# Kernel optimization log

Hardware: AMD Instinct MI355X
Metric: run time of the kernel (lower is better)

The kernel has to match this reference:

```python
import jax, jax.numpy as jnp
import numpy as np

NQ, NS, D, DC, HT = 100000, 2000, 128, 64, 128
B, T = 128, 500
NNZ_HG, NNZ_GCN, NNZ_SIM = 300000, 64000, 1000000
NUM_MV, NUM_QL = 2, 2


def spmm(rows, cols, vals, x, n_rows):
    # y = A @ x, A sparse COO with A[rows[k], cols[k]] = vals[k]
    return jax.ops.segment_sum(vals[:, None] * x[cols], rows, num_segments=n_rows)


def gcn_conv(x, src, dst, W, b, n):
    # PyG-style GCNConv: sym-normalized (A + I), then linear + bias
    h = x @ W
    loop = jnp.arange(n, dtype=src.dtype)
    s = jnp.concatenate([src, loop])
    d = jnp.concatenate([dst, loop])
    deg = jax.ops.segment_sum(jnp.ones(s.shape[0], jnp.float32), d, num_segments=n)
    dinv = jax.lax.rsqrt(jnp.maximum(deg, 1.0))
    norm = dinv[s] * dinv[d]
    return jax.ops.segment_sum(norm[:, None] * h[s], d, num_segments=n) + b


def setup_inputs() -> dict:
    key = jax.random.key(0)
    ks = iter(jax.random.split(key, 64))
    nrm = lambda shape, s=0.05: jax.random.normal(next(ks), shape, jnp.float32) * s
    ri = lambda shape, hi: jax.random.randint(next(ks), shape, 0, hi, jnp.int32)
    inp = {}
    inp['question_seq'] = ri((B, T), NQ)
    inp['skill_seq'] = ri((B, T), NS)
    inp['answer_seq'] = ri((B, T), 2)
    inp['hg_q'] = ri((NNZ_HG,), NQ)
    inp['hg_c'] = ri((NNZ_HG,), NS)
    inp['gcn_src'] = ri((NNZ_GCN,), NS)
    inp['gcn_dst'] = ri((NNZ_GCN,), NS)
    inp['sim_src'] = ri((NNZ_SIM,), NQ)
    inp['sim_dst'] = ri((NNZ_SIM,), NQ)
    inp['hg_vals_qc'] = jax.random.uniform(next(ks), (NNZ_HG,), jnp.float32) * 0.05
    inp['hg_vals_cq'] = jax.random.uniform(next(ks), (NNZ_HG,), jnp.float32) * 0.05
    inp['sim_vals'] = jax.random.uniform(next(ks), (NNZ_SIM,), jnp.float32) * 0.02
    inp['q_emb'] = nrm((NQ + 1, D))
    inp['s_emb'] = nrm((NS + 1, D))
    inp['c_emb'] = nrm((3, DC))
    for nm in ['w_g1', 'w_g2', 'w_g3']:
        inp[nm] = nrm((D, D))
    for nm in ['b_g1', 'b_g2', 'b_g3']:
        inp[nm] = nrm((1, D))
    for i in [1, 2, 3]:
        inp['gcn_w%d' % i] = nrm((D, D))
        inp['gcn_b%d' % i] = nrm((D,))
    for nm in ['w_sg1', 'w_sg2', 'w_qg1', 'w_qg3']:
        inp[nm] = nrm((D, 1))
    for nm in ['b_sg1', 'b_sg2', 'b_qg1', 'b_qg3']:
        inp[nm] = nrm((1,))
    LIN = 2 * D + DC
    inp['w_ih'] = nrm((4 * HT, LIN))
    inp['w_hh'] = nrm((4 * HT, HT))
    inp['b_ih'] = nrm((4 * HT,))
    inp['b_hh'] = nrm((4 * HT,))
    inp['fc1_w'] = nrm((HT + 2 * D, HT))
    inp['fc1_b'] = nrm((HT,))
    inp['fc2_w'] = nrm((HT, 1))
    inp['fc2_b'] = nrm((1,))
    return inp


def reference(question_seq, skill_seq, answer_seq, hg_q, hg_c, gcn_src, gcn_dst,
              sim_src, sim_dst, hg_vals_qc, hg_vals_cq, sim_vals,
              q_emb, s_emb, c_emb, w_g1, w_g2, w_g3, b_g1, b_g2, b_g3,
              gcn_w1, gcn_b1, gcn_w2, gcn_b2, gcn_w3, gcn_b3,
              w_sg1, w_sg2, w_qg1, w_qg3, b_sg1, b_sg2, b_qg1, b_qg3,
              w_ih, w_hh, b_ih, b_hh, fc1_w, fc1_b, fc2_w, fc2_b):
    sig = jax.nn.sigmoid
    # gated (channel-specific) embedding tables, excluding padding row
    one_gate = s_emb[:-1] * sig(s_emb[:-1] @ w_g1 + b_g1)
    two_gate = s_emb[:-1] * sig(s_emb[:-1] @ w_g2 + b_g2)
    three_gate = q_emb[:-1] * sig(q_emb[:-1] @ w_g3 + b_g3)

    # channel 1: multi-view hypergraph conv with residual + mean over layers (dropout p=0 -> identity)
    embs = [one_gate]
    x = one_gate
    for _ in range(NUM_MV):
        m = spmm(hg_q, hg_c, hg_vals_qc, x, NQ)   # HG_qc @ x -> [NQ, D]
        x = spmm(hg_c, hg_q, hg_vals_cq, m, NS)   # HG_cq @ m -> [NS, D]
        x = x + embs[-1]
        embs.append(x)
    one_skill = jnp.mean(jnp.stack(embs), 0)
    one_q = spmm(hg_q, hg_c, hg_vals_qc, one_skill, NQ)  # structural question embs
    one_skill_p = jnp.concatenate([one_skill, s_emb[-1:]], 0)
    one_q_p = jnp.concatenate([one_q, q_emb[-1:]], 0)
    one_b_skill = one_skill_p[skill_seq]   # [B,T,D]
    one_b_q = one_q_p[question_seq]        # [B,T,D]

    # channel 2: 3-layer GCN with relu (dropout p=0)
    x = jax.nn.relu(gcn_conv(two_gate, gcn_src, gcn_dst, gcn_w1, gcn_b1, NS))
    x = jax.nn.relu(gcn_conv(x, gcn_src, gcn_dst, gcn_w2, gcn_b2, NS))
    x = jax.nn.relu(gcn_conv(x, gcn_src, gcn_dst, gcn_w3, gcn_b3, NS))
    two_skill_p = jnp.concatenate([x, s_emb[-1:]], 0)
    two_b_skill = two_skill_p[skill_seq]

    # channel 3: question similarity conv with residual + mean over layers
    embs = [three_gate]
    x = three_gate
    for _ in range(NUM_QL):
        x = spmm(sim_src, sim_dst, sim_vals, x, NQ) + embs[-1]
        embs.append(x)
    three_q = jnp.mean(jnp.stack(embs), 0)
    three_q_p = jnp.concatenate([three_q, q_emb[-1:]], 0)
    three_b_q = three_q_p[question_seq]

    # gated channel fusion
    fused_skill = sig(one_b_skill @ w_sg1 + b_sg1) * one_b_skill \
                + sig(two_b_skill @ w_sg2 + b_sg2) * two_b_skill
    fused_q = sig(one_b_q @ w_qg1 + b_qg1) * one_b_q \
            + sig(three_b_q @ w_qg3 + b_qg3) * three_b_q
    corr = c_emb[answer_seq]  # [B,T,DC]
    lstm_in = jnp.concatenate([fused_q, fused_skill, corr], -1)  # [B,T,2D+DC]

    def step(carry, xt):
        h, c = carry
        z = xt @ w_ih.T + b_ih + h @ w_hh.T + b_hh
        i, f, g, o = jnp.split(z, 4, axis=-1)  # torch LSTM gate order
        c = sig(f) * c + sig(i) * jnp.tanh(g)
        h = sig(o) * jnp.tanh(c)
        return (h, c), h

    b = lstm_in.shape[0]
    h0 = jnp.zeros((b, HT), lstm_in.dtype)
    _, hs = jax.lax.scan(step, (h0, h0), jnp.swapaxes(lstm_in, 0, 1))
    hs = jnp.swapaxes(hs, 0, 1)  # [B,T,HT]

    pred_in = jnp.concatenate([hs, fused_q, fused_skill], -1)  # [B,T,HT+2D]
    preds = sig(jax.nn.relu(pred_in @ fc1_w + fc1_b) @ fc2_w + fc2_b)  # [B,T,1]
    return preds
```

## Files before the change

kernel.cpp:

```cpp
#include <hip/hip_runtime.h>

#define NQc 100000
#define NSc 2000
#define Dc 128
#define DCc 64
#define HTc 128
#define Bc 128
#define Tc 500
#define BTc (Bc*Tc)
#define NNZ_HGc 300000
#define NNZ_GCNc 64000
#define NNZ_SIMc 1000000
#define LINc 320
#define G4c 512

using bf16x8  = __attribute__((ext_vector_type(8))) short;
using floatx4 = __attribute__((ext_vector_type(4))) float;
typedef _Float16 half2v __attribute__((ext_vector_type(2)));

__device__ __forceinline__ float sigf(float x){ return 1.0f/(1.0f + __expf(-x)); }
__device__ __forceinline__ float tanhfast(float x){ return 2.0f*sigf(2.0f*x) - 1.0f; }

__device__ __forceinline__ unsigned short bf16r(float x){
  unsigned u = __float_as_uint(x);
// ... 10 lines not shown
  #pragma unroll
  for (int off=32; off>0; off>>=1) v += __shfl_xor(v, off, 64);
  return v;
}

__global__ void fill_kernel(float* p, float v, int n){
  int i = blockIdx.x*blockDim.x + threadIdx.x;
  if (i<n) p[i] = v;
}

__global__ void cvt_bf16_kernel(const float* __restrict__ in, unsigned short* __restrict__ out, long n){
  long i = (long)blockIdx.x*blockDim.x + threadIdx.x;
  long stride = (long)gridDim.x*blockDim.x;
  for (; i<n; i+=stride) out[i] = bf16r(in[i]);
}
__global__ void cvtT_bf16_kernel(const float* __restrict__ in, unsigned short* __restrict__ out, int R, int C){
  int i = blockIdx.x*blockDim.x + threadIdx.x;
  if (i < R*C){ int r = i/C, c = i%C; out[(size_t)c*R + r] = bf16r(in[i]); }
}
__global__ void cvt_f16_kernel(const float* __restrict__ in, _Float16* __restrict__ out, int n){
  int i = blockIdx.x*blockDim.x + threadIdx.x;
  if (i<n) out[i] = (_Float16)in[i];
}
__global__ void cvtP_wih_kernel(const float* __restrict__ in, unsigned short* __restrict__ out){
  int i = blockIdx.x*blockDim.x + threadIdx.x;
  if (i < G4c*LINc){
    int r = i/LINc, c = i%LINc;
    int rp = (r&127)*4 + (r>>7);
    out[(size_t)rp*LINc + c] = bf16r(in[i]);
  }
}
__global__ void biasP_kernel(const float* __restrict__ bih, const float* __restrict__ bhh, float* __restrict__ out){
  int r = blockIdx.x*blockDim.x + threadIdx.x;
  if (r < G4c) out[(r&127)*4 + (r>>7)] = bih[r] + bhh[r];
}

__global__ void hist_kernel(const int* __restrict__ rows, int* cnt, int nnz){
  int i = blockIdx.x*blockDim.x + threadIdx.x;
  int stride = gridDim.x*blockDim.x;
  for (; i<nnz; i+=stride) atomicAdd(&cnt[rows[i]], 1);
}

__global__ __launch_bounds__(1024) void scan_local_kernel(const int* __restrict__ cnt, int* __restrict__ rowptr,
                                                          int* __restrict__ bsum, int n){
  __shared__ int buf[1024];
  int tid = threadIdx.x;
  int i = blockIdx.x*1024 + tid;
  int v = (i<n) ? cnt[i] : 0;
  buf[tid] = v;
  __syncthreads();
  for (int off=1; off<1024; off<<=1){
    int t = (tid>=off) ? buf[tid-off] : 0;
    __syncthreads();
    buf[tid] += t;
    __syncthreads();
  }
  if (i<n) rowptr[i] = buf[tid] - v;
  if (tid==1023) bsum[blockIdx.x] = buf[1023];
}
__global__ __launch_bounds__(128) void scan_bsum_kernel(int* bsum, int nb){
  __shared__ int s[128];
  int tid = threadIdx.x;
  int v = (tid<nb) ? bsum[tid] : 0;
  s[tid] = v;
  __syncthreads();
  for (int off=1; off<128; off<<=1){
    int t = (tid>=off) ? s[tid-off] : 0;
    __syncthreads();
    s[tid] += t;
    __syncthreads();
  }
  if (tid<nb) bsum[tid] = s[tid] - v;
  if (tid==0) bsum[nb] = s[127];
}
__global__ void scan_add_kernel(int* rowptr, int* cur, const int* __restrict__ bsum, int n, int nb){
  int i = blockIdx.x*blockDim.x + threadIdx.x;
  if (i<n){ int r = rowptr[i] + bsum[i>>10]; rowptr[i]=r; cur[i]=r; }
  if (i==0) rowptr[n] = bsum[nb];
}

__global__ void scatter_kernel(const int* __restrict__ rows, const int* __restrict__ cols,
                               const float* __restrict__ vals, int* cur,
                               int* col_out, float* val_out, int nnz){
  int i = blockIdx.x*blockDim.x + threadIdx.x;
  int stride = gridDim.x*blockDim.x;
  for (; i<nnz; i+=stride){
    int r = rows[i];
    int p = atomicAdd(&cur[r], 1);
    col_out[p] = cols[i];
    if (vals) val_out[p] = vals[i];
  }
}

__global__ void dinv_kernel(const int* __restrict__ cnt, float* dinv, int n){
  int i = blockIdx.x*blockDim.x + threadIdx.x;
  if (i<n) dinv[i] = rsqrtf((float)cnt[i] + 1.0f);
}

__global__ void copy_kernel(float* __restrict__ dst, const float* __restrict__ src, long n4){
  long i = (long)blockIdx.x*blockDim.x + threadIdx.x;
  long stride = (long)gridDim.x*blockDim.x;
  const float4* s = (const float4*)src; float4* d = (float4*)dst;
  for (; i<n4; i+=stride) d[i] = s[i];
}

#define BM 64
#define BN 64
#define BK 16
__global__ __launch_bounds__(256) void gemm_kernel(
    const float* __restrict__ A, int lda,
    const float* __restrict__ Bm, float* __restrict__ C,
    const float* __restrict__ bias, const float* __restrict__ gsrc,
    int M, int N, int K, int ep)
{
  __shared__ float As[BM][BK+4];
  __shared__ float Bs[BK][BN+4];
  int tid = threadIdx.x;
  int tx = tid & 15, ty = tid >> 4;
  int mBase = blockIdx.y*BM, nBase = blockIdx.x*BN;
  float acc[4][4];
  #pragma unroll
  for (int i=0;i<4;i++)
    #pragma unroll
    for (int j=0;j<4;j++) acc[i][j]=0.f;
  int arow = tid>>2, ac4 = tid&3;
  for (int kt=0; kt<K; kt+=BK){
// ... 19 lines not shown
      acc[3][0]+=a3*b0; acc[3][1]+=a3*b1; acc[3][2]+=a3*b2; acc[3][3]+=a3*b3;
    }
    __syncthreads();
  }
  #pragma unroll
  for (int i=0;i<4;i++){
    int m = mBase + ty*4 + i;
    if (m >= M) continue;
    #pragma unroll
    for (int j=0;j<4;j++){
      int n = nBase + tx*4 + j;
      float v = acc[i][j];
      if (bias)  v += bias[n];
      if (ep==1)      v = gsrc[(size_t)m*N + n] * sigf(v);
      C[(size_t)m*N + n] = v;
    }
  }
}

__global__ __launch_bounds__(256) void mfma_gemm_kernel(
    const unsigned short* __restrict__ A1, int lda1,
    const unsigned short* __restrict__ A2, int lda2, int ksplit,
    const unsigned short* __restrict__ Bt,
    float* __restrict__ C, unsigned short* __restrict__ Cbf,
    const float* __restrict__ bias, const float* __restrict__ bias2,
    const float* __restrict__ gsrc,
    int M, int N, int K, int ep)
{
  __shared__ unsigned short Asm[128*64];
  __shared__ unsigned short Bsm[128*64];
  int tid = threadIdx.x;
  int wave = tid>>6, lane = tid&63;
  int quad = lane>>4, l16 = lane&15;
  int m0 = blockIdx.y*128, n0 = blockIdx.x*128;
  int wm = (wave&1)*64, wn = (wave>>1)*64;
  floatx4 acc[4][4];
  #pragma unroll
  for (int i=0;i<4;i++)
    #pragma unroll
    for (int j=0;j<4;j++) acc[i][j] = (floatx4){0.f,0.f,0.f,0.f};

  for (int kt=0; kt<K; kt+=64){
    #pragma unroll
    for (int i=0;i<4;i++){
      int idx = i*256 + tid;
// ... 24 lines not shown
      }
      #pragma unroll
      for (int nt=0;nt<4;nt++){
        int row = wn + nt*16 + l16;
        int blk = ks*4 + quad;
        bfr[nt] = *(const bf16x8*)&Bsm[row*64 + ((blk ^ (row&7))<<3)];
      }
      #pragma unroll
      for (int mt=0;mt<4;mt++)
        #pragma unroll
        for (int nt=0;nt<4;nt++)
          acc[mt][nt] = __builtin_amdgcn_mfma_f32_16x16x32_bf16(af[mt], bfr[nt], acc[mt][nt], 0,0,0);
    }
    __syncthreads();
  }
  #pragma unroll
  for (int mt=0;mt<4;mt++){
    #pragma unroll
    for (int nt=0;nt<4;nt++){
      int col = n0 + wn + nt*16 + l16;
      #pragma unroll
      for (int r=0;r<4;r++){
        int row = m0 + wm + mt*16 + quad*4 + r;
        if (row < M){
          float v = acc[mt][nt][r];
          if (bias)  v += bias[col];
          if (bias2) v += bias2[col];
          if (ep==1)      v = gsrc[(size_t)row*N + col] * sigf(v);
          else if (ep==2) v = fmaxf(v, 0.f);
          C[(size_t)row*N + col] = v;
          if (Cbf) Cbf[(size_t)row*N + col] = bf16r(v);
        }
      }
    }
  }
}

__global__ __launch_bounds__(256) void spmm_bf_kernel(
    const int* __restrict__ rowptr, const int* __restrict__ col, const float* __restrict__ val,
    const unsigned short* __restrict__ xbf, const float* __restrict__ resid,
    const float* __restrict__ resid2, float beta,
    float* __restrict__ y, unsigned short* __restrict__ ybf, float* __restrict__ sumbuf,
    float alpha, int nrows)
{
  int w = (int)((blockIdx.x*(unsigned)blockDim.x + threadIdx.x) >> 6);
  int lane = threadIdx.x & 63;
  if (w >= nrows) return;
  int beg = rowptr[w], end = rowptr[w+1];
  const unsigned* x2 = (const unsigned*)xbf;
  float ax=0.f, ay=0.f;
  int k = beg;
  for (; k+4 <= end; k+=4){
    int c0=col[k], c1=col[k+1], c2=col[k+2], c3=col[k+3];
    float v0=val[k], v1=val[k+1], v2=val[k+2], v3=val[k+3];
    unsigned u0 = x2[(size_t)c0*64 + lane];
    unsigned u1 = x2[(size_t)c1*64 + lane];
    unsigned u2 = x2[(size_t)c2*64 + lane];
// ... 6 lines not shown
  for (; k<end; k++){
    int c = col[k]; float v = val[k];
    unsigned u = x2[(size_t)c*64 + lane];
    ax += v*bflo(u); ay += v*bfhi(u);
  }
  ax*=alpha; ay*=alpha;
  if (resid){ float2 r = ((const float2*)resid)[(size_t)w*64+lane]; ax+=r.x; ay+=r.y; }
  if (resid2){ float2 r = ((const float2*)resid2)[(size_t)w*64+lane]; ax+=beta*r.x; ay+=beta*r.y; }
  float2 o; o.x=ax; o.y=ay;
  ((float2*)y)[(size_t)w*64+lane] = o;
  if (ybf) ((unsigned*)ybf)[(size_t)w*64+lane] = pack2(o);
  if (sumbuf){
    float2 s = ((float2*)sumbuf)[(size_t)w*64+lane];
    s.x+=ax; s.y+=ay;
    ((float2*)sumbuf)[(size_t)w*64+lane] = s;
  }
}

__global__ __launch_bounds__(256) void gcn_spmm_kernel(
    const int* __restrict__ rowptr, const int* __restrict__ src, const float* __restrict__ dinv,
    const float* __restrict__ h, const float* __restrict__ bias, float* __restrict__ out, int nrows)
{
  int w = (int)((blockIdx.x*(unsigned)blockDim.x + threadIdx.x) >> 6);
  int lane = threadIdx.x & 63;
  if (w >= nrows) return;
  int beg = rowptr[w], end = rowptr[w+1];
  const float2* h2 = (const float2*)h;
  float dr = dinv[w];
  float2 self = h2[(size_t)w*64+lane];
  float ax = dr*self.x, ay = dr*self.y;
// ... 68 lines not shown
  rowb[lane]      = pack2(fq);
  rowb[64 + lane] = pack2(fs);
  if (lane < 32){
    float2 cv = ((const float2*)(c_emb + (size_t)a*DCc))[lane];
    rowb[128 + lane] = pack2(cv);
  }
}

__global__ __launch_bounds__(512, 2) void lstm_kernel(
    const float* __restrict__ xpart, const _Float16* __restrict__ w_hh_h,
    unsigned short* __restrict__ hs_bf)
{
  __shared__ __align__(16) _Float16 h_lds[2][HTc];
  int b = blockIdx.x, tid = threadIdx.x;
  int j = tid >> 2, sub = tid & 3;
  half2v w[4][16];
  #pragma unroll
  for (int g=0; g<4; g++){
    const half2v* wp = (const half2v*)(w_hh_h + (size_t)(g*128 + j)*HTc + sub*32);
    #pragma unroll
    for (int i=0;i<16;i++) w[g][i] = wp[i];
  }
  if (tid < HTc) h_lds[0][tid] = (_Float16)0.f;
  float c = 0.f;
  __syncthreads();
  const float* xp = xpart + (size_t)b*Tc*G4c;
  unsigned short* hb = hs_bf + (size_t)b*Tc*HTc;
  float xcur = xp[tid];
  for (int t=0; t<Tc; t++){
    int tn = (t+1 < Tc) ? t+1 : Tc-1;
    float xnext = xp[(size_t)tn*G4c + tid];
    int cur = t & 1;
    float4 hv[4];
    const float4* hsrc = (const float4*)&h_lds[cur][sub*32];
    #pragma unroll
    for (int i=0;i<4;i++) hv[i] = hsrc[i];
    const half2v* hh = (const half2v*)hv;
    float p0=0.f,p1=0.f,p2=0.f,p3=0.f;
    #pragma unroll
    for (int i=0;i<16;i++){
#if __has_builtin(__builtin_amdgcn_fdot2)
      p0 = __builtin_amdgcn_fdot2(w[0][i], hh[i], p0, false);
      p1 = __builtin_amdgcn_fdot2(w[1][i], hh[i], p1, false);
      p2 = __builtin_amdgcn_fdot2(w[2][i], hh[i], p2, false);
      p3 = __builtin_amdgcn_fdot2(w[3][i], hh[i], p3, false);
#else
      p0 += (float)w[0][i].x*(float)hh[i].x + (float)w[0][i].y*(float)hh[i].y;
      p1 += (float)w[1][i].x*(float)hh[i].x + (float)w[1][i].y*(float)hh[i].y;
      p2 += (float)w[2][i].x*(float)hh[i].x + (float)w[2][i].y*(float)hh[i].y;
      p3 += (float)w[3][i].x*(float)hh[i].x + (float)w[3][i].y*(float)hh[i].y;
#endif
    }
    if (sub==0) p0 += xcur; else if (sub==1) p1 += xcur; else if (sub==2) p2 += xcur; else p3 += xcur;
    p0 += __shfl_xor(p0,1); p0 += __shfl_xor(p0,2);
    p1 += __shfl_xor(p1,1); p1 += __shfl_xor(p1,2);
    p2 += __shfl_xor(p2,1); p2 += __shfl_xor(p2,2);
    p3 += __shfl_xor(p3,1); p3 += __shfl_xor(p3,2);
    float ig=sigf(p0), fg=sigf(p1), gg=tanhfast(p2), og=sigf(p3);
    c = fg*c + ig*gg;
    float h = og*tanhfast(c);
    if (sub == 0){
      h_lds[1-cur][j] = (_Float16)h;
      hb[(size_t)t*HTc + j] = bf16r(h);
    }
    __syncthreads();
    xcur = xnext;
  }
}

__global__ __launch_bounds__(256) void final_kernel(
    const float* __restrict__ h1, const float* __restrict__ fc2_w,
    const float* __restrict__ fc2_b, float* __restrict__ out){
  int idx = (int)((blockIdx.x*(unsigned)blockDim.x + threadIdx.x) >> 6);
  int lane = threadIdx.x & 63;
  if (idx >= BTc) return;
  float2 h = ((const float2*)(h1 + (size_t)idx*HTc))[lane];
  float2 w = ((const float2*)fc2_w)[lane];
  float p = wredsum(h.x*w.x + h.y*w.y);
  if (lane==0) out[idx] = sigf(p + fc2_b[0]);
}

extern "C" void kernel_launch(void* const* d_in, const int* in_sizes, int n_in,
                              void* d_out, int out_size, void* d_ws, size_t ws_size,
                              hipStream_t stream)
{
  const int* question_seq=(const int*)d_in[0];
  const int* skill_seq   =(const int*)d_in[1];
  const int* answer_seq  =(const int*)d_in[2];
  const int* hg_q        =(const int*)d_in[3];
  const int* hg_c        =(const int*)d_in[4];
  const int* gcn_src     =(const int*)d_in[5];
  const int* gcn_dst     =(const int*)d_in[6];
  const int* sim_src     =(const int*)d_in[7];
  const int* sim_dst     =(const int*)d_in[8];
// ... 63 lines not shown
  size_t p_val_sim = pall((size_t)NNZ_SIMc*4);
  size_t p_col_hgq = pall((size_t)NNZ_HGc*4);
  size_t p_val_hgq = pall((size_t)NNZ_HGc*4);
  size_t p_col_hgc = pall((size_t)NNZ_HGc*4);
  size_t p_val_hgc = pall((size_t)NNZ_HGc*4);
  size_t p_src_gcn = pall((size_t)NNZ_GCNc*4);
  size_t p_rp_sim  = pall((size_t)(NQc+1)*4);
  size_t p_rp_hgq  = pall((size_t)(NQc+1)*4);
  size_t p_rp_hgc  = pall((size_t)(NSc+1)*4);
  size_t p_rp_gcn  = pall((size_t)(NSc+1)*4);
  size_t p_cnt_sim = pall((size_t)NQc*4);
  size_t p_cnt_hgq = pall((size_t)NQc*4);
  size_t p_cnt_hgc = pall((size_t)NSc*4);
  size_t p_cnt_gcn = pall((size_t)NSc*4);
  size_t p_cnt_end = poff;
  size_t p_bsum    = pall((size_t)130*4);
  size_t p_dinv    = pall((size_t)NSc*4);
  size_t p_onegate = pall((size_t)NSc*Dc*4);
  size_t p_twogate = pall((size_t)NSc*Dc*4);
  size_t p_ssum    = pall((size_t)NSc*Dc*4);
  size_t p_sxA     = pall((size_t)NSc*Dc*4);
  size_t p_sxB     = pall((size_t)NSc*Dc*4);
  size_t p_gxA     = pall((size_t)NSc*Dc*4);
  size_t p_gxB     = pall((size_t)NSc*Dc*4);
  size_t p_htmp    = pall((size_t)NSc*Dc*4);
  size_t p_ogbf    = pall((size_t)NSc*Dc*2);
  size_t p_sxBbf   = pall((size_t)NSc*Dc*2);
  size_t p_ssumbf  = pall((size_t)NSc*Dc*2);
  if (poff > XPbytes){
    fill_kernel<<<(out_size+255)/256, 256, 0, stream>>>(outp, -2.0f, out_size);
    return;
// ... 19 lines not shown
  int*   bsum    = (int*)(xp + p_bsum);
  float* dinv    = (float*)(xp + p_dinv);
  float* one_gate= (float*)(xp + p_onegate);
  float* two_gate= (float*)(xp + p_twogate);
  float* ssum    = (float*)(xp + p_ssum);
  float* sxA     = (float*)(xp + p_sxA);
  float* sxB     = (float*)(xp + p_sxB);
  float* gxA     = (float*)(xp + p_gxA);
  float* gxB     = (float*)(xp + p_gxB);
  float* htmp    = (float*)(xp + p_htmp);
  unsigned short* og_bf   = (unsigned short*)(xp + p_ogbf);
  unsigned short* sxB_bf  = (unsigned short*)(xp + p_sxBbf);
  unsigned short* ssum_bf = (unsigned short*)(xp + p_ssumbf);

  float* xpart   = (float*)xp;
  float* h1buf   = (float*)xp;
  unsigned short* lstm_in_bf = (unsigned short*)(base + o_libf);
  unsigned short* hs_bf      = (unsigned short*)(base + o_hsbf);
  unsigned short* q_emb_bf   = (unsigned short*)(base + o_qembbf);
  unsigned short* bfX        = (unsigned short*)(base + o_qembbf);
  unsigned short* bfY        = (unsigned short*)(base + o_bfY);
  unsigned short* w_ih_bf    = (unsigned short*)(base + o_wihbf);
  unsigned short* fc1_wT     = (unsigned short*)(base + o_fc1wT);
  unsigned short* w_g3T      = (unsigned short*)(base + o_wg3T);
  _Float16*       w_hh_h     = (_Float16*)(base + o_whhh);
  float*          biasP      = (float*)(base + o_biasP);

  auto gemm32 = [&](const float* A, int lda, const float* Bp, float* Cp, const float* bias,
                    const float* gsrc, int M, int N, int K, int ep){
    dim3 g(N/64, (M+63)/64), b(256);
    gemm_kernel<<<g, b, 0, stream>>>(A, lda, Bp, Cp, bias, gsrc, M, N, K, ep);
  };
  auto spmm = [&](const int* rp, const int* col, const float* val, const unsigned short* xb,
                  const float* resid, const float* resid2, float beta,
                  float* y, unsigned short* yb, float* sum, float alpha, int nrows){
    spmm_bf_kernel<<<(nrows+3)/4, 256, 0, stream>>>(rp, col, val, xb, resid, resid2, beta, y, yb, sum, alpha, nrows);
  };
  auto scan = [&](int* cnt, int* rowptr, int n){
    int nb = (n + 1023)/1024;
    scan_local_kernel<<<nb, 1024, 0, stream>>>(cnt, rowptr, bsum, n);
    scan_bsum_kernel<<<1, 128, 0, stream>>>(bsum, nb);
    scan_add_kernel<<<(n+255)/256, 256, 0, stream>>>(rowptr, cnt, bsum, n, nb);
  };

  hipMemsetAsync(xp + p_cnt_sim, 0, p_cnt_end - p_cnt_sim, stream);
  hist_kernel<<<1024, 256, 0, stream>>>(sim_src, cnt_sim, NNZ_SIMc);
  hist_kernel<<<1024, 256, 0, stream>>>(hg_q,    cnt_hgq, NNZ_HGc);
  hist_kernel<<<1024, 256, 0, stream>>>(hg_c,    cnt_hgc, NNZ_HGc);
  hist_kernel<<<256,  256, 0, stream>>>(gcn_dst, cnt_gcn, NNZ_GCNc);
  dinv_kernel<<<(NSc+255)/256, 256, 0, stream>>>(cnt_gcn, dinv, NSc);
  scan(cnt_sim, rp_sim, NQc);
  scan(cnt_hgq, rp_hgq, NQc);
  scan(cnt_hgc, rp_hgc, NSc);
  scan(cnt_gcn, rp_gcn, NSc);
  scatter_kernel<<<1024, 256, 0, stream>>>(sim_src, sim_dst, sim_vals, cnt_sim, col_sim, val_sim, NNZ_SIMc);
  scatter_kernel<<<1024, 256, 0, stream>>>(hg_q, hg_c, hg_vals_qc, cnt_hgq, col_hgq, val_hgq, NNZ_HGc);
  scatter_kernel<<<1024, 256, 0, stream>>>(hg_c, hg_q, hg_vals_cq, cnt_hgc, col_hgc, val_hgc, NNZ_HGc);
  scatter_kernel<<<256,  256, 0, stream>>>(gcn_dst, gcn_src, nullptr, cnt_gcn, src_gcn, nullptr, NNZ_GCNc);

  cvt_bf16_kernel<<<2048, 256, 0, stream>>>(q_emb, q_emb_bf, (long)(NQc+1)*Dc);
  cvtP_wih_kernel<<<(G4c*LINc+255)/256, 256, 0, stream>>>(w_ih, w_ih_bf);
  biasP_kernel<<<2, 256, 0, stream>>>(b_ih, b_hh, biasP);
  cvtT_bf16_kernel<<<(384*HTc+255)/256, 256, 0, stream>>>(fc1_w, fc1_wT, 384, HTc);
  cvtT_bf16_kernel<<<(Dc*Dc+255)/256, 256, 0, stream>>>(w_g3, w_g3T, Dc, Dc);
  cvt_f16_kernel<<<(G4c*HTc+255)/256, 256, 0, stream>>>(w_hh, w_hh_h, G4c*HTc);

  {
    dim3 g(1, (NQc+127)/128);
    mfma_gemm_kernel<<<g, 256, 0, stream>>>(q_emb_bf, Dc, q_emb_bf, Dc, Dc, w_g3T,
                                            Abuf, bfY, b_g3, nullptr, q_emb, NQc, Dc, Dc, 1);
  }
  spmm(rp_sim, col_sim, val_sim, bfY, Abuf, nullptr, 0.f, Bbuf, bfX,    nullptr, 1.f, NQc);
  spmm(rp_sim, col_sim, val_sim, bfX, Abuf, Bbuf, 2.f,   Abuf, nullptr, nullptr, 1.f, NQc);

  gemm32(s_emb, Dc, w_g1, one_gate, b_g1, s_emb, NSc, Dc, Dc, 1);
  gemm32(s_emb, Dc, w_g2, two_gate, b_g2, s_emb, NSc, Dc, Dc, 1);
  cvt_bf16_kernel<<<500, 256, 0, stream>>>(one_gate, og_bf, (long)NSc*Dc);

  copy_kernel<<<256, 256, 0, stream>>>(ssum, one_gate, (long)NSc*Dc/4);
  spmm(rp_hgq, col_hgq, val_hgq, og_bf,  nullptr, nullptr, 0.f, Bbuf, bfY,     nullptr, 1.f, NQc);
  spmm(rp_hgc, col_hgc, val_hgc, bfY,    one_gate, nullptr, 0.f, sxB,  sxB_bf,  ssum,    1.f, NSc);
  spmm(rp_hgq, col_hgq, val_hgq, sxB_bf, nullptr, nullptr, 0.f, Bbuf, bfY,     nullptr, 1.f, NQc);
  spmm(rp_hgc, col_hgc, val_hgc, bfY,    sxB,     nullptr, 0.f, sxA,  nullptr, ssum,    1.f, NSc);
  cvt_bf16_kernel<<<500, 256, 0, stream>>>(ssum, ssum_bf, (long)NSc*Dc);
  spmm(rp_hgq, col_hgq, val_hgq, ssum_bf, nullptr, nullptr, 0.f, Bbuf, nullptr, nullptr, 1.f/3.f, NQc);

  gemm32(two_gate, Dc, gcn_w1, htmp, nullptr, nullptr, NSc, Dc, Dc, 0);
  gcn_spmm_kernel<<<(NSc+3)/4, 256, 0, stream>>>(rp_gcn, src_gcn, dinv, htmp, gcn_b1, gxA, NSc);
  gemm32(gxA, Dc, gcn_w2, htmp, nullptr, nullptr, NSc, Dc, Dc, 0);
  gcn_spmm_kernel<<<(NSc+3)/4, 256, 0, stream>>>(rp_gcn, src_gcn, dinv, htmp, gcn_b2, gxB, NSc);
  gemm32(gxB, Dc, gcn_w3, htmp, nullptr, nullptr, NSc, Dc, Dc, 0);
  gcn_spmm_kernel<<<(NSc+3)/4, 256, 0, stream>>>(rp_gcn, src_gcn, dinv, htmp, gcn_b3, gxA, NSc);

  gather_fuse_kernel<<<(BTc+3)/4, 256, 0, stream>>>(
      question_seq, skill_seq, answer_seq,
      ssum, Bbuf, gxA, Abuf,
      s_emb, q_emb, c_emb,
      w_sg1, w_sg2, w_qg1, w_qg3, b_sg1, b_sg2, b_qg1, b_qg3,
      lstm_in_bf);

  {
    dim3 g(G4c/128, BTc/128);
    mfma_gemm_kernel<<<g, 256, 0, stream>>>(lstm_in_bf, LINc, lstm_in_bf, LINc, LINc, w_ih_bf,
                                            xpart, nullptr, biasP, nullptr, nullptr, BTc, G4c, LINc, 0);
  }

  lstm_kernel<<<Bc, 512, 0, stream>>>(xpart, w_hh_h, hs_bf);

  {
    dim3 g(1, BTc/128);
    mfma_gemm_kernel<<<g, 256, 0, stream>>>(hs_bf, HTc, lstm_in_bf, LINc, HTc, fc1_wT,
                                            h1buf, nullptr, fc1_b, nullptr, nullptr, BTc, HTc, 384, 2);
  }
  final_kernel<<<(BTc+3)/4, 256, 0, stream>>>(h1buf, fc2_w, fc2_b, outp);
}
```

Before: 1.503 ms.

## Batch preprocessing kernels, fuse fc2 into fc1 GEMM epilogue, pin LSTM weights

```diff
diff --git a/kernel.cpp b/kernel.cpp
--- a/kernel.cpp
+++ b/kernel.cpp
@@ -48,39 +48,73 @@
   long stride = (long)gridDim.x*blockDim.x;
   for (; i<n; i+=stride) out[i] = bf16r(in[i]);
 }
-__global__ void cvtT_bf16_kernel(const float* __restrict__ in, unsigned short* __restrict__ out, int R, int C){
+
+__global__ void cvt_weights_kernel(
+    const float* __restrict__ w_ih, unsigned short* __restrict__ w_ih_bf,
+    const float* __restrict__ fc1_w, unsigned short* __restrict__ fc1_wT,
+    const float* __restrict__ w_g3, unsigned short* __restrict__ w_g3T,
+    const float* __restrict__ w_hh, _Float16* __restrict__ w_hh_h,
+    const float* __restrict__ b_ih, const float* __restrict__ b_hh, float* __restrict__ biasP)
+{
   int i = blockIdx.x*blockDim.x + threadIdx.x;
-  if (i < R*C){ int r = i/C, c = i%C; out[(size_t)c*R + r] = bf16r(in[i]); }
-}
-__global__ void cvt_f16_kernel(const float* __restrict__ in, _Float16* __restrict__ out, int n){
-  int i = blockIdx.x*blockDim.x + threadIdx.x;
-  if (i<n) out[i] = (_Float16)in[i];
-}
-__global__ void cvtP_wih_kernel(const float* __restrict__ in, unsigned short* __restrict__ out){
-  int i = blockIdx.x*blockDim.x + threadIdx.x;
-  if (i < G4c*LINc){
+  const int T0 = G4c*LINc;
+  const int T1 = T0 + 384*HTc;
+  const int T2 = T1 + Dc*Dc;
+  const int T3 = T2 + G4c*HTc;
+  const int T4 = T3 + G4c;
+  if (i < T0){
     int r = i/LINc, c = i%LINc;
     int rp = (r&127)*4 + (r>>7);
-    out[(size_t)rp*LINc + c] = bf16r(in[i]);
-  }
-}
-__global__ void biasP_kernel(const float* __restrict__ bih, const float* __restrict__ bhh, float* __restrict__ out){
-  int r = blockIdx.x*blockDim.x + threadIdx.x;
-  if (r < G4c) out[(r&127)*4 + (r>>7)] = bih[r] + bhh[r];
-}
-
-__global__ void hist_kernel(const int* __restrict__ rows, int* cnt, int nnz){
-  int i = blockIdx.x*blockDim.x + threadIdx.x;
-  int stride = gridDim.x*blockDim.x;
-  for (; i<nnz; i+=stride) atomicAdd(&cnt[rows[i]], 1);
-}
-
-__global__ __launch_bounds__(1024) void scan_local_kernel(const int* __restrict__ cnt, int* __restrict__ rowptr,
-                                                          int* __restrict__ bsum, int n){
+    w_ih_bf[(size_t)rp*LINc + c] = bf16r(w_ih[i]);
+  } else if (i < T1){
+    int j = i - T0; int r = j/HTc, c = j%HTc;
+    fc1_wT[(size_t)c*384 + r] = bf16r(fc1_w[j]);
+  } else if (i < T2){
+    int j = i - T1; int r = j/Dc, c = j%Dc;
+    w_g3T[(size_t)c*Dc + r] = bf16r(w_g3[j]);
+  } else if (i < T3){
+    int j = i - T2;
+    w_hh_h[j] = (_Float16)w_hh[j];
+  } else if (i < T4){
+    int j = i - T3;
+    biasP[(j&127)*4 + (j>>7)] = b_ih[j] + b_hh[j];
+  }
+}
+
+__global__ void hist_all_kernel(const int* __restrict__ sim_src, int* cnt_sim,
+                                const int* __restrict__ hg_q, int* cnt_hgq,
+                                const int* __restrict__ hg_c, int* cnt_hgc,
+                                const int* __restrict__ gcn_dst, int* cnt_gcn){
+  long i = (long)blockIdx.x*blockDim.x + threadIdx.x;
+  long stride = (long)gridDim.x*blockDim.x;
+  const long T0=NNZ_SIMc, T1=T0+NNZ_HGc, T2=T1+NNZ_HGc, T3=T2+NNZ_GCNc;
+  for (; i<T3; i+=stride){
+    if (i<T0)      atomicAdd(&cnt_sim[sim_src[i]], 1);
+    else if (i<T1) atomicAdd(&cnt_hgq[hg_q[i-T0]], 1);
+    else if (i<T2) atomicAdd(&cnt_hgc[hg_c[i-T1]], 1);
+    else           atomicAdd(&cnt_gcn[gcn_dst[i-T2]], 1);
+  }
+}
+
+#define BS_STRIDE 104
+__global__ __launch_bounds__(1024) void scan_local_all_kernel(
+    const int* __restrict__ cnt_sim, int* rp_sim,
+    const int* __restrict__ cnt_hgq, int* rp_hgq,
+    const int* __restrict__ cnt_hgc, int* rp_hgc,
+    const int* __restrict__ cnt_gcn, int* rp_gcn,
+    int* __restrict__ bsum, float* __restrict__ dinv)
+{
   __shared__ int buf[1024];
-  int tid = threadIdx.x;
-  int i = blockIdx.x*1024 + tid;
+  int b = blockIdx.x, tid = threadIdx.x;
+  const int* cnt; int* rp; int* bs; int n; int lb; int seg;
+  if (b < 98)      { seg=0; cnt=cnt_sim; rp=rp_sim; n=NQc; lb=b; }
+  else if (b <196) { seg=1; cnt=cnt_hgq; rp=rp_hgq; n=NQc; lb=b-98; }
+  else if (b <198) { seg=2; cnt=cnt_hgc; rp=rp_hgc; n=NSc; lb=b-196; }
+  else             { seg=3; cnt=cnt_gcn; rp=rp_gcn; n=NSc; lb=b-198; }
+  bs = bsum + seg*BS_STRIDE;
+  int i = lb*1024 + tid;
   int v = (i<n) ? cnt[i] : 0;
+  if (seg==3 && i<n) dinv[i] = rsqrtf((float)v + 1.0f);
   buf[tid] = v;
   __syncthreads();
   for (int off=1; off<1024; off<<=1){
@@ -89,13 +123,15 @@
     buf[tid] += t;
     __syncthreads();
   }
-  if (i<n) rowptr[i] = buf[tid] - v;
-  if (tid==1023) bsum[blockIdx.x] = buf[1023];
-}
-__global__ __launch_bounds__(128) void scan_bsum_kernel(int* bsum, int nb){
+  if (i<n) rp[i] = buf[tid] - v;
+  if (tid==1023) bs[lb] = buf[1023];
+}
+__global__ __launch_bounds__(128) void scan_bsum_all_kernel(int* bsum){
   __shared__ int s[128];
-  int tid = threadIdx.x;
-  int v = (tid<nb) ? bsum[tid] : 0;
+  int seg = blockIdx.x, tid = threadIdx.x;
+  int nb = (seg<2) ? 98 : 2;
+  int* bs = bsum + seg*BS_STRIDE;
+  int v = (tid<nb) ? bs[tid] : 0;
   s[tid] = v;
   __syncthreads();
   for (int off=1; off<128; off<<=1){
@@ -104,38 +140,53 @@
     s[tid] += t;
     __syncthreads();
   }
-  if (tid<nb) bsum[tid] = s[tid] - v;
-  if (tid==0) bsum[nb] = s[127];
-}
-__global__ void scan_add_kernel(int* rowptr, int* cur, const int* __restrict__ bsum, int n, int nb){
-  int i = blockIdx.x*blockDim.x + threadIdx.x;
-  if (i<n){ int r = rowptr[i] + bsum[i>>10]; rowptr[i]=r; cur[i]=r; }
-  if (i==0) rowptr[n] = bsum[nb];
-}
-
-__global__ void scatter_kernel(const int* __restrict__ rows, const int* __restrict__ cols,
-                               const float* __restrict__ vals, int* cur,
-                               int* col_out, float* val_out, int nnz){
-  int i = blockIdx.x*blockDim.x + threadIdx.x;
-  int stride = gridDim.x*blockDim.x;
-  for (; i<nnz; i+=stride){
-    int r = rows[i];
-    int p = atomicAdd(&cur[r], 1);
-    col_out[p] = cols[i];
-    if (vals) val_out[p] = vals[i];
-  }
-}
-
-__global__ void dinv_kernel(const int* __restrict__ cnt, float* dinv, int n){
-  int i = blockIdx.x*blockDim.x + threadIdx.x;
-  if (i<n) dinv[i] = rsqrtf((float)cnt[i] + 1.0f);
-}
-
-__global__ void copy_kernel(float* __restrict__ dst, const float* __restrict__ src, long n4){
+  if (tid<nb) bs[tid] = s[tid] - v;
+  if (tid==0) bs[nb] = s[127];
+}
+__global__ void scan_add_all_kernel(
+    int* rp_sim, int* cnt_sim, int* rp_hgq, int* cnt_hgq,
+    int* rp_hgc, int* cnt_hgc, int* rp_gcn, int* cnt_gcn,
+    const int* __restrict__ bsum)
+{
+  int b = blockIdx.x, tid = threadIdx.x;
+  int* rp; int* cur; const int* bs; int n; int lb; int nb;
+  if (b < 391)      { rp=rp_sim; cur=cnt_sim; bs=bsum;               n=NQc; lb=b;     nb=98; }
+  else if (b < 782) { rp=rp_hgq; cur=cnt_hgq; bs=bsum+BS_STRIDE;     n=NQc; lb=b-391; nb=98; }
+  else if (b < 790) { rp=rp_hgc; cur=cnt_hgc; bs=bsum+2*BS_STRIDE;   n=NSc; lb=b-782; nb=2; }
+  else              { rp=rp_gcn; cur=cnt_gcn; bs=bsum+3*BS_STRIDE;   n=NSc; lb=b-790; nb=2; }
+  int i = lb*256 + tid;
+  if (i<n){ int r = rp[i] + bs[i>>10]; rp[i]=r; cur[i]=r; }
+  if (lb==0 && tid==0) rp[n] = bs[nb];
+}
+
+__global__ void scatter_all_kernel(
+    const int* __restrict__ sim_src, const int* __restrict__ sim_dst, const float* __restrict__ sim_vals,
+    int* cur_sim, int* col_sim, float* val_sim,
+    const int* __restrict__ hg_q, const int* __restrict__ hg_c,
+    const float* __restrict__ hg_vals_qc, const float* __restrict__ hg_vals_cq,
+    int* cur_hgq, int* col_hgq, float* val_hgq,
+    int* cur_hgc, int* col_hgc, float* val_hgc,
+    const int* __restrict__ gcn_dst, const int* __restrict__ gcn_src,
+    int* cur_gcn, int* src_gcn)
+{
   long i = (long)blockIdx.x*blockDim.x + threadIdx.x;
   long stride = (long)gridDim.x*blockDim.x;
-  const float4* s = (const float4*)src; float4* d = (float4*)dst;
-  for (; i<n4; i+=stride) d[i] = s[i];
+  const long T0=NNZ_SIMc, T1=T0+NNZ_HGc, T2=T1+NNZ_HGc, T3=T2+NNZ_GCNc;
+  for (; i<T3; i+=stride){
+    if (i<T0){
+      int r = sim_src[i]; int p = atomicAdd(&cur_sim[r],1);
+      col_sim[p] = sim_dst[i]; val_sim[p] = sim_vals[i];
+    } else if (i<T1){
+      long j=i-T0; int r = hg_q[j]; int p = atomicAdd(&cur_hgq[r],1);
+      col_hgq[p] = hg_c[j]; val_hgq[p] = hg_vals_qc[j];
+    } else if (i<T2){
+      long j=i-T1; int r = hg_c[j]; int p = atomicAdd(&cur_hgc[r],1);
+      col_hgc[p] = hg_q[j]; val_hgc[p] = hg_vals_cq[j];
+    } else {
+      long j=i-T2; int r = gcn_dst[j]; int p = atomicAdd(&cur_gcn[r],1);
+      src_gcn[p] = gcn_src[j];
+    }
+  }
 }
 
 #define BM 64
@@ -144,6 +195,7 @@
 __global__ __launch_bounds__(256) void gemm_kernel(
     const float* __restrict__ A, int lda,
     const float* __restrict__ Bm, float* __restrict__ C,
+    unsigned short* __restrict__ Cbf, float* __restrict__ Ccopy,
     const float* __restrict__ bias, const float* __restrict__ gsrc,
     int M, int N, int K, int ep)
 {
@@ -193,6 +245,8 @@
       if (bias)  v += bias[n];
       if (ep==1)      v = gsrc[(size_t)m*N + n] * sigf(v);
       C[(size_t)m*N + n] = v;
+      if (Cbf)   Cbf[(size_t)m*N + n] = bf16r(v);
+      if (Ccopy) Ccopy[(size_t)m*N + n] = v;
     }
   }
 }
@@ -204,10 +258,12 @@
     float* __restrict__ C, unsigned short* __restrict__ Cbf,
     const float* __restrict__ bias, const float* __restrict__ bias2,
     const float* __restrict__ gsrc,
+    const float* __restrict__ fc2w, const float* __restrict__ fc2b, float* __restrict__ outp,
     int M, int N, int K, int ep)
 {
   __shared__ unsigned short Asm[128*64];
   __shared__ unsigned short Bsm[128*64];
+  __shared__ float rps[2][128];
   int tid = threadIdx.x;
   int wave = tid>>6, lane = tid&63;
   int quad = lane>>4, l16 = lane&15;
@@ -262,6 +318,32 @@
     }
     __syncthreads();
   }
+  if (ep == 3){
+    float fw[4], fb[4];
+    #pragma unroll
+    for (int nt=0;nt<4;nt++){ int col = wn + nt*16 + l16; fw[nt] = fc2w[col]; fb[nt] = bias[col]; }
+    #pragma unroll
+    for (int mt=0;mt<4;mt++){
+      #pragma unroll
+      for (int r=0;r<4;r++){
+        float s = 0.f;
+        #pragma unroll
+        for (int nt=0;nt<4;nt++){
+          float v = acc[mt][nt][r] + fb[nt];
+          v = fmaxf(v, 0.f);
+          s += v*fw[nt];
+        }
+        s += __shfl_xor(s,1); s += __shfl_xor(s,2); s += __shfl_xor(s,4); s += __shfl_xor(s,8);
+        if (l16 == 0) rps[wave>>1][wm + mt*16 + quad*4 + r] = s;
+      }
+    }
+    __syncthreads();
+    if (tid < 128){
+      int row = m0 + tid;
+      if (row < M) outp[row] = sigf(rps[0][tid] + rps[1][tid] + fc2b[0]);
+    }
+    return;
+  }
   #pragma unroll
   for (int mt=0;mt<4;mt++){
     #pragma unroll
@@ -288,7 +370,8 @@
     const int* __restrict__ rowptr, const int* __restrict__ col, const float* __restrict__ val,
     const unsigned short* __restrict__ xbf, const float* __restrict__ resid,
     const float* __restrict__ resid2, float beta,
-    float* __restrict__ y, unsigned short* __restrict__ ybf, float* __restrict__ sumbuf,
+    float* __restrict__ y, unsigned short* __restrict__ ybf,
+    float* __restrict__ sumbuf, unsigned short* __restrict__ sumbf,
     float alpha, int nrows)
 {
   int w = (int)((blockIdx.x*(unsigned)blockDim.x + threadIdx.x) >> 6);
@@ -325,6 +408,7 @@
     float2 s = ((float2*)sumbuf)[(size_t)w*64+lane];
     s.x+=ax; s.y+=ay;
     ((float2*)sumbuf)[(size_t)w*64+lane] = s;
+    if (sumbf) ((unsigned*)sumbf)[(size_t)w*64+lane] = pack2(s);
   }
 }
 
@@ -423,13 +507,18 @@
   __shared__ __align__(16) _Float16 h_lds[2][HTc];
   int b = blockIdx.x, tid = threadIdx.x;
   int j = tid >> 2, sub = tid & 3;
-  half2v w[4][16];
+  unsigned wbits[4][16];
   #pragma unroll
   for (int g=0; g<4; g++){
-    const half2v* wp = (const half2v*)(w_hh_h + (size_t)(g*128 + j)*HTc + sub*32);
-    #pragma unroll
-    for (int i=0;i<16;i++) w[g][i] = wp[i];
-  }
+    const unsigned* wp = (const unsigned*)(w_hh_h + (size_t)(g*128 + j)*HTc + sub*32);
+    #pragma unroll
+    for (int i=0;i<16;i++) wbits[g][i] = wp[i];
+  }
+  #pragma unroll
+  for (int g=0; g<4; g++)
+    #pragma unroll
+    for (int i=0;i<16;i++)
+      asm volatile("" : "+v"(wbits[g][i]));
   if (tid < HTc) h_lds[0][tid] = (_Float16)0.f;
   float c = 0.f;
   __syncthreads();
@@ -448,16 +537,21 @@
     float p0=0.f,p1=0.f,p2=0.f,p3=0.f;
     #pragma unroll
     for (int i=0;i<16;i++){
+      half2v h2 = hh[i];
 #if __has_builtin(__builtin_amdgcn_fdot2)
-      p0 = __builtin_amdgcn_fdot2(w[0][i], hh[i], p0, false);
-      p1 = __builtin_amdgcn_fdot2(w[1][i], hh[i], p1, false);
-      p2 = __builtin_amdgcn_fdot2(w[2][i], hh[i], p2, false);
-      p3 = __builtin_amdgcn_fdot2(w[3][i], hh[i], p3, false);
+      p0 = __builtin_amdgcn_fdot2(__builtin_bit_cast(half2v, wbits[0][i]), h2, p0, false);
+      p1 = __builtin_amdgcn_fdot2(__builtin_bit_cast(half2v, wbits[1][i]), h2, p1, false);
+      p2 = __builtin_amdgcn_fdot2(__builtin_bit_cast(half2v, wbits[2][i]), h2, p2, false);
+      p3 = __builtin_amdgcn_fdot2(__builtin_bit_cast(half2v, wbits[3][i]), h2, p3, false);
 #else
-      p0 += (float)w[0][i].x*(float)hh[i].x + (float)w[0][i].y*(float)hh[i].y;
-      p1 += (float)w[1][i].x*(float)hh[i].x + (float)w[1][i].y*(float)hh[i].y;
-      p2 += (float)w[2][i].x*(float)hh[i].x + (float)w[2][i].y*(float)hh[i].y;
-      p3 += (float)w[3][i].x*(float)hh[i].x + (float)w[3][i].y*(float)hh[i].y;
+      half2v w0 = __builtin_bit_cast(half2v, wbits[0][i]);
+      half2v w1 = __builtin_bit_cast(half2v, wbits[1][i]);
+      half2v w2 = __builtin_bit_cast(half2v, wbits[2][i]);
+      half2v w3 = __builtin_bit_cast(half2v, wbits[3][i]);
+      p0 += (float)w0.x*(float)h2.x + (float)w0.y*(float)h2.y;
+      p1 += (float)w1.x*(float)h2.x + (float)w1.y*(float)h2.y;
+      p2 += (float)w2.x*(float)h2.x + (float)w2.y*(float)h2.y;
+      p3 += (float)w3.x*(float)h2.x + (float)w3.y*(float)h2.y;
 #endif
     }
     if (sub==0) p0 += xcur; else if (sub==1) p1 += xcur; else if (sub==2) p2 += xcur; else p3 += xcur;
@@ -475,18 +569,6 @@
     __syncthreads();
     xcur = xnext;
   }
-}
-
-__global__ __launch_bounds__(256) void final_kernel(
-    const float* __restrict__ h1, const float* __restrict__ fc2_w,
-    const float* __restrict__ fc2_b, float* __restrict__ out){
-  int idx = (int)((blockIdx.x*(unsigned)blockDim.x + threadIdx.x) >> 6);
-  int lane = threadIdx.x & 63;
-  if (idx >= BTc) return;
-  float2 h = ((const float2*)(h1 + (size_t)idx*HTc))[lane];
-  float2 w = ((const float2*)fc2_w)[lane];
-  float p = wredsum(h.x*w.x + h.y*w.y);
-  if (lane==0) out[idx] = sigf(p + fc2_b[0]);
 }
 
 extern "C" void kernel_launch(void* const* d_in, const int* in_sizes, int n_in,
@@ -580,7 +662,7 @@
   size_t p_cnt_hgc = pall((size_t)NSc*4);
   size_t p_cnt_gcn = pall((size_t)NSc*4);
   size_t p_cnt_end = poff;
-  size_t p_bsum    = pall((size_t)130*4);
+  size_t p_bsum    = pall((size_t)4*BS_STRIDE*4);
   size_t p_dinv    = pall((size_t)NSc*4);
   size_t p_onegate = pall((size_t)NSc*Dc*4);
   size_t p_twogate = pall((size_t)NSc*Dc*4);
@@ -630,7 +712,6 @@
   unsigned short* ssum_bf = (unsigned short*)(xp + p_ssumbf);
 
   float* xpart   = (float*)xp;
-  float* h1buf   = (float*)xp;
   unsigned short* lstm_in_bf = (unsigned short*)(base + o_libf);
   unsigned short* hs_bf      = (unsigned short*)(base + o_hsbf);
   unsigned short* q_emb_bf   = (unsigned short*)(base + o_qembbf);
@@ -642,70 +723,59 @@
   _Float16*       w_hh_h     = (_Float16*)(base + o_whhh);
   float*          biasP      = (float*)(base + o_biasP);
 
-  auto gemm32 = [&](const float* A, int lda, const float* Bp, float* Cp, const float* bias,
+  auto gemm32 = [&](const float* A, int lda, const float* Bp, float* Cp,
+                    unsigned short* Cbf, float* Ccopy, const float* bias,
                     const float* gsrc, int M, int N, int K, int ep){
     dim3 g(N/64, (M+63)/64), b(256);
-    gemm_kernel<<<g, b, 0, stream>>>(A, lda, Bp, Cp, bias, gsrc, M, N, K, ep);
+    gemm_kernel<<<g, b, 0, stream>>>(A, lda, Bp, Cp, Cbf, Ccopy, bias, gsrc, M, N, K, ep);
   };
   auto spmm = [&](const int* rp, const int* col, const float* val, const unsigned short* xb,
                   const float* resid, const float* resid2, float beta,
-                  float* y, unsigned short* yb, float* sum, float alpha, int nrows){
-    spmm_bf_kernel<<<(nrows+3)/4, 256, 0, stream>>>(rp, col, val, xb, resid, resid2, beta, y, yb, sum, alpha, nrows);
+                  float* y, unsigned short* yb, float* sum, unsigned short* sumbf,
+                  float alpha, int nrows){
+    spmm_bf_kernel<<<(nrows+3)/4, 256, 0, stream>>>(rp, col, val, xb, resid, resid2, beta, y, yb, sum, sumbf, alpha, nrows);
   };
-  auto scan = [&](int* cnt, int* rowptr, int n){
-    int nb = (n + 1023)/1024;
-    scan_local_kernel<<<nb, 1024, 0, stream>>>(cnt, rowptr, bsum, n);
-    scan_bsum_kernel<<<1, 128, 0, stream>>>(bsum, nb);
-    scan_add_kernel<<<(n+255)/256, 256, 0, stream>>>(rowptr, cnt, bsum, n, nb);
-  };
 
   hipMemsetAsync(xp + p_cnt_sim, 0, p_cnt_end - p_cnt_sim, stream);
-  hist_kernel<<<1024, 256, 0, stream>>>(sim_src, cnt_sim, NNZ_SIMc);
-  hist_kernel<<<1024, 256, 0, stream>>>(hg_q,    cnt_hgq, NNZ_HGc);
-  hist_kernel<<<1024, 256, 0, stream>>>(hg_c,    cnt_hgc, NNZ_HGc);
-  hist_kernel<<<256,  256, 0, stream>>>(gcn_dst, cnt_gcn, NNZ_GCNc);
-  dinv_kernel<<<(NSc+255)/256, 256, 0, stream>>>(cnt_gcn, dinv, NSc);
-  scan(cnt_sim, rp_sim, NQc);
-  scan(cnt_hgq, rp_hgq, NQc);
-  scan(cnt_hgc, rp_hgc, NSc);
-  scan(cnt_gcn, rp_gcn, NSc);
-  scatter_kernel<<<1024, 256, 0, stream>>>(sim_src, sim_dst, sim_vals, cnt_sim, col_sim, val_sim, NNZ_SIMc);
-  scatter_kernel<<<1024, 256, 0, stream>>>(hg_q, hg_c, hg_vals_qc, cnt_hgq, col_hgq, val_hgq, NNZ_HGc);
-  scatter_kernel<<<1024, 256, 0, stream>>>(hg_c, hg_q, hg_vals_cq, cnt_hgc, col_hgc, val_hgc, NNZ_HGc);
-  scatter_kernel<<<256,  256, 0, stream>>>(gcn_dst, gcn_src, nullptr, cnt_gcn, src_gcn, nullptr, NNZ_GCNc);
+  hist_all_kernel<<<2048, 256, 0, stream>>>(sim_src, cnt_sim, hg_q, cnt_hgq, hg_c, cnt_hgc, gcn_dst, cnt_gcn);
+  scan_local_all_kernel<<<200, 1024, 0, stream>>>(cnt_sim, rp_sim, cnt_hgq, rp_hgq,
+                                                  cnt_hgc, rp_hgc, cnt_gcn, rp_gcn, bsum, dinv);
+  scan_bsum_all_kernel<<<4, 128, 0, stream>>>(bsum);
+  scan_add_all_kernel<<<798, 256, 0, stream>>>(rp_sim, cnt_sim, rp_hgq, cnt_hgq,
+                                               rp_hgc, cnt_hgc, rp_gcn, cnt_gcn, bsum);
+  scatter_all_kernel<<<2048, 256, 0, stream>>>(
+      sim_src, sim_dst, sim_vals, cnt_sim, col_sim, val_sim,
+      hg_q, hg_c, hg_vals_qc, hg_vals_cq,
+      cnt_hgq, col_hgq, val_hgq, cnt_hgc, col_hgc, val_hgc,
+      gcn_dst, gcn_src, cnt_gcn, src_gcn);
 
   cvt_bf16_kernel<<<2048, 256, 0, stream>>>(q_emb, q_emb_bf, (long)(NQc+1)*Dc);
-  cvtP_wih_kernel<<<(G4c*LINc+255)/256, 256, 0, stream>>>(w_ih, w_ih_bf);
-  biasP_kernel<<<2, 256, 0, stream>>>(b_ih, b_hh, biasP);
-  cvtT_bf16_kernel<<<(384*HTc+255)/256, 256, 0, stream>>>(fc1_w, fc1_wT, 384, HTc);
-  cvtT_bf16_kernel<<<(Dc*Dc+255)/256, 256, 0, stream>>>(w_g3, w_g3T, Dc, Dc);
-  cvt_f16_kernel<<<(G4c*HTc+255)/256, 256, 0, stream>>>(w_hh, w_hh_h, G4c*HTc);
+  cvt_weights_kernel<<<1154, 256, 0, stream>>>(w_ih, w_ih_bf, fc1_w, fc1_wT, w_g3, w_g3T,
+                                               w_hh, w_hh_h, b_ih, b_hh, biasP);
 
   {
     dim3 g(1, (NQc+127)/128);
     mfma_gemm_kernel<<<g, 256, 0, stream>>>(q_emb_bf, Dc, q_emb_bf, Dc, Dc, w_g3T,
-                                            Abuf, bfY, b_g3, nullptr, q_emb, NQc, Dc, Dc, 1);
-  }
-  spmm(rp_sim, col_sim, val_sim, bfY, Abuf, nullptr, 0.f, Bbuf, bfX,    nullptr, 1.f, NQc);
-  spmm(rp_sim, col_sim, val_sim, bfX, Abuf, Bbuf, 2.f,   Abuf, nullptr, nullptr, 1.f, NQc);
-
-  gemm32(s_emb, Dc, w_g1, one_gate, b_g1, s_emb, NSc, Dc, Dc, 1);
-  gemm32(s_emb, Dc, w_g2, two_gate, b_g2, s_emb, NSc, Dc, Dc, 1);
-  cvt_bf16_kernel<<<500, 256, 0, stream>>>(one_gate, og_bf, (long)NSc*Dc);
-
-  copy_kernel<<<256, 256, 0, stream>>>(ssum, one_gate, (long)NSc*Dc/4);
-  spmm(rp_hgq, col_hgq, val_hgq, og_bf,  nullptr, nullptr, 0.f, Bbuf, bfY,     nullptr, 1.f, NQc);
-  spmm(rp_hgc, col_hgc, val_hgc, bfY,    one_gate, nullptr, 0.f, sxB,  sxB_bf,  ssum,    1.f, NSc);
-  spmm(rp_hgq, col_hgq, val_hgq, sxB_bf, nullptr, nullptr, 0.f, Bbuf, bfY,     nullptr, 1.f, NQc);
-  spmm(rp_hgc, col_hgc, val_hgc, bfY,    sxB,     nullptr, 0.f, sxA,  nullptr, ssum,    1.f, NSc);
-  cvt_bf16_kernel<<<500, 256, 0, stream>>>(ssum, ssum_bf, (long)NSc*Dc);
-  spmm(rp_hgq, col_hgq, val_hgq, ssum_bf, nullptr, nullptr, 0.f, Bbuf, nullptr, nullptr, 1.f/3.f, NQc);
-
-  gemm32(two_gate, Dc, gcn_w1, htmp, nullptr, nullptr, NSc, Dc, Dc, 0);
+                                            Abuf, bfY, b_g3, nullptr, q_emb,
+                                            nullptr, nullptr, nullptr, NQc, Dc, Dc, 1);
+  }
+  spmm(rp_sim, col_sim, val_sim, bfY, Abuf, nullptr, 0.f, Bbuf, bfX,    nullptr, nullptr, 1.f, NQc);
+  spmm(rp_sim, col_sim, val_sim, bfX, Abuf, Bbuf, 2.f,   Abuf, nullptr, nullptr, nullptr, 1.f, NQc);
+
+  gemm32(s_emb, Dc, w_g1, one_gate, og_bf, ssum, b_g1, s_emb, NSc, Dc, Dc, 1);
+  gemm32(s_emb, Dc, w_g2, two_gate, nullptr, nullptr, b_g2, s_emb, NSc, Dc, Dc, 1);
+
+  spmm(rp_hgq, col_hgq, val_hgq, og_bf,  nullptr,  nullptr, 0.f, Bbuf, bfY,    nullptr, nullptr, 1.f, NQc);
+  spmm(rp_hgc, col_hgc, val_hgc, bfY,    one_gate, nullptr, 0.f, sxB,  sxB_bf, ssum,    nullptr, 1.f, NSc);
+  spmm(rp_hgq, col_hgq, val_hgq, sxB_bf, nullptr,  nullptr, 0.f, Bbuf, bfY,    nullptr, nullptr, 1.f, NQc);
+  spmm(rp_hgc, col_hgc, val_hgc, bfY,    sxB,      nullptr, 0.f, sxA,  nullptr, ssum,   ssum_bf, 1.f, NSc);
+  spmm(rp_hgq, col_hgq, val_hgq, ssum_bf, nullptr, nullptr, 0.f, Bbuf, nullptr, nullptr, nullptr, 1.f/3.f, NQc);
+
+  gemm32(two_gate, Dc, gcn_w1, htmp, nullptr, nullptr, nullptr, nullptr, NSc, Dc, Dc, 0);
   gcn_spmm_kernel<<<(NSc+3)/4, 256, 0, stream>>>(rp_gcn, src_gcn, dinv, htmp, gcn_b1, gxA, NSc);
-  gemm32(gxA, Dc, gcn_w2, htmp, nullptr, nullptr, NSc, Dc, Dc, 0);
+  gemm32(gxA, Dc, gcn_w2, htmp, nullptr, nullptr, nullptr, nullptr, NSc, Dc, Dc, 0);
   gcn_spmm_kernel<<<(NSc+3)/4, 256, 0, stream>>>(rp_gcn, src_gcn, dinv, htmp, gcn_b2, gxB, NSc);
-  gemm32(gxB, Dc, gcn_w3, htmp, nullptr, nullptr, NSc, Dc, Dc, 0);
+  gemm32(gxB, Dc, gcn_w3, htmp, nullptr, nullptr, nullptr, nullptr, NSc, Dc, Dc, 0);
   gcn_spmm_kernel<<<(NSc+3)/4, 256, 0, stream>>>(rp_gcn, src_gcn, dinv, htmp, gcn_b3, gxA, NSc);
 
   gather_fuse_kernel<<<(BTc+3)/4, 256, 0, stream>>>(
@@ -718,7 +788,8 @@
   {
     dim3 g(G4c/128, BTc/128);
     mfma_gemm_kernel<<<g, 256, 0, stream>>>(lstm_in_bf, LINc, lstm_in_bf, LINc, LINc, w_ih_bf,
-                                            xpart, nullptr, biasP, nullptr, nullptr, BTc, G4c, LINc, 0);
+                                            xpart, nullptr, biasP, nullptr, nullptr,
+                                            nullptr, nullptr, nullptr, BTc, G4c, LINc, 0);
   }
 
   lstm_kernel<<<Bc, 512, 0, stream>>>(xpart, w_hh_h, hs_bf);
@@ -726,7 +797,7 @@
   {
     dim3 g(1, BTc/128);
     mfma_gemm_kernel<<<g, 256, 0, stream>>>(hs_bf, HTc, lstm_in_bf, LINc, HTc, fc1_wT,
-                                            h1buf, nullptr, fc1_b, nullptr, nullptr, BTc, HTc, 384, 2);
-  }
-  final_kernel<<<(BTc+3)/4, 256, 0, stream>>>(h1buf, fc2_w, fc2_b, outp);
-}
+                                            nullptr, nullptr, fc1_b, nullptr, nullptr,
+                                            fc2_w, fc2_b, outp, BTc, 128, 384, 3);
+  }
+}
```

After: 1.407 ms. -6.3%, faster.
